# Kernel tuning notes

Measured on AMD Instinct MI355X. Metric: run time of the kernel, lower is better.

Reference implementation:

```python
import jax, jax.numpy as jnp
import numpy as np
from jax import lax

RADIUS = 32
STRIDE = RADIUS // 2
EPS = 1e-4
DN = ('NCHW', 'OIHW', 'NCHW')


def _upsample_bilinear_ac(x, H, W):
    # align_corners=True bilinear resize of NCHW x to (H, W), separable gather.
    b, c, h, w = x.shape
    ys = jnp.linspace(0.0, h - 1, H)
    xs = jnp.linspace(0.0, w - 1, W)
    y0 = jnp.floor(ys).astype(jnp.int32)
    y1 = jnp.minimum(y0 + 1, h - 1)
    wy = (ys - y0.astype(x.dtype)).astype(x.dtype)
    x0 = jnp.floor(xs).astype(jnp.int32)
    x1 = jnp.minimum(x0 + 1, w - 1)
    wx = (xs - x0.astype(x.dtype)).astype(x.dtype)
    rows = x[:, :, y0, :] * (1 - wy)[None, None, :, None] + x[:, :, y1, :] * wy[None, None, :, None]
    out = rows[:, :, :, x0] * (1 - wx) + rows[:, :, :, x1] * wx
    return out


def reference(guide, src, w1, w3):
    B, _, H, W = guide.shape
    f32 = guide.dtype

    def box3(x):  # depthwise strided box-sum (all-ones weights)
        return lax.conv_general_dilated(x, w3, (STRIDE, STRIDE), 'VALID',
                                        dimension_numbers=DN, feature_group_count=3)

    def box1(x):  # learned 1-channel strided conv
        return lax.conv_general_dilated(x, w1, (STRIDE, STRIDE), 'VALID',
                                        dimension_numbers=DN)

    gr, gg, gb = guide[:, 0:1], guide[:, 1:2], guide[:, 2:3]
    N = box1(jnp.ones_like(gr))                     # [B,1,h,w]
    mean_I = box3(guide) / N                        # [B,3,h,w]
    mIr, mIg, mIb = mean_I[:, 0:1], mean_I[:, 1:2], mean_I[:, 2:3]
    mean_p = box3(src) / N                          # [B,3,h,w]

    cov_r = box3(gr * src) / N - mIr * mean_p       # [B,3,h,w]
    cov_g = box3(gg * src) / N - mIg * mean_p
    cov_b = box3(gb * src) / N - mIb * mean_p

    v_rr = box1(gr * gr) / N - mIr * mIr + EPS
    v_rg = box1(gr * gg) / N - mIr * mIg
    v_rb = box1(gr * gb) / N - mIr * mIb
    v_gg = box1(gg * gg) / N - mIg * mIg + EPS
    v_gb = box1(gg * gb) / N - mIg * mIb
    v_bb = box1(gb * gb) / N - mIb * mIb + EPS

    det = (v_rr * v_gg * v_bb + v_rg * v_gb * v_rb + v_rb * v_rg * v_gb
           - v_rb * v_gg * v_rb - v_rg * v_rg * v_bb - v_rr * v_gb * v_gb)

    i_rr = (v_gg * v_bb - v_gb * v_gb) / det
    i_rg = -(v_rg * v_bb - v_rb * v_gb) / det
    i_rb = (v_rg * v_gb - v_rb * v_gg) / det
    i_gg = (v_rr * v_bb - v_rb * v_rb) / det
    i_gb = -(v_rr * v_gb - v_rb * v_rg) / det
    i_bb = (v_rr * v_gg - v_rg * v_rg) / det

    # inv_sigma: [B,3,3,h,w] (each i_* is [B,1,h,w] -> concat on channel)
    row_r = jnp.concatenate([i_rr, i_rg, i_rb], axis=1)
    row_g = jnp.concatenate([i_rg, i_gg, i_gb], axis=1)
    row_b = jnp.concatenate([i_rb, i_gb, i_bb], axis=1)
    inv_sigma = jnp.stack([row_r, row_g, row_b], axis=1)

    cov_Ip = jnp.stack([cov_r, cov_g, cov_b], axis=1)   # [B,3(i),3(c),h,w]
    A = jnp.einsum('bichw,bijhw->bjchw', cov_Ip, inv_sigma)  # [B,3(j),3(c),h,w]

    b_map = mean_p - A[:, 0] * mIr - A[:, 1] * mIg - A[:, 2] * mIb  # [B,3,h,w]

    h, w = A.shape[-2], A.shape[-1]
    mean_A = _upsample_bilinear_ac(A.reshape(B, 9, h, w), H, W).reshape(B, 3, 3, H, W)
    mean_b = _upsample_bilinear_ac(b_map, H, W)

    # q_c = sum_j A_{j,c} * guide_j + b_c
    return jnp.einsum('bjchw,bjhw->bchw', mean_A, guide) + mean_b


def setup_inputs() -> dict:
    key = jax.random.key(0)
    k1, k2, k3 = jax.random.split(key, 3)
    guide = jax.random.uniform(k1, (8, 3, 1024, 1024), dtype=jnp.float32)
    src = jax.random.uniform(k2, (8, 3, 1024, 1024), dtype=jnp.float32)
    w1 = jax.random.uniform(k3, (1, 1, RADIUS, RADIUS), dtype=jnp.float32)
    w3 = jnp.ones((3, 1, RADIUS, RADIUS), dtype=jnp.float32)
    return {"guide": guide, "src": src, "w1": w1, "w3": w3}
```

## Files before the change

### kernel.cpp

```cpp
#include <hip/hip_runtime.h>

#define HLO 63
#define HFULL 1024
#define GF_EPS 1e-4f
#define LOPLANE (HLO*HLO)
#define NQ 64
#define NSTAT 40

template<int CTRL>
__device__ __forceinline__ float dppadd(float v) {
    int r = __builtin_amdgcn_update_dpp(0, __float_as_int(v), CTRL, 0xF, 0xF, false);
    return v + __int_as_float(r);
}

__global__ __launch_bounds__(256) void gf_vstats(
    const float* __restrict__ guide, const float* __restrict__ src,
    const float* __restrict__ w1, float* __restrict__ hs)
{
    __shared__ float red[4][NSTAT][4];

    int bid = blockIdx.x;
    int cg = bid & 15;
    int qy = (bid >> 4) & 63;
    int b  = bid >> 10;
    int tid = threadIdx.x;
    int lane = tid & 63;
    int wv   = tid >> 6;

    int r   = lane & 3;
    int c4  = lane >> 2;
    int xin = (c4 & 3) * 4;
    int yin = wv * 4 + r;

    const size_t plane = (size_t)HFULL * HFULL;
    const float* g0 = guide + (size_t)b * 3 * plane
                    + (size_t)(qy * 16 + yin) * HFULL + cg * 64 + c4 * 4;
    const float* s0 = src   + (size_t)b * 3 * plane
                    + (size_t)(qy * 16 + yin) * HFULL + cg * 64 + c4 * 4;

    float4 vgr = *reinterpret_cast<const float4*>(g0);
    float4 vgg = *reinterpret_cast<const float4*>(g0 + plane);
    float4 vgb = *reinterpret_cast<const float4*>(g0 + 2 * plane);
    float4 vpr = *reinterpret_cast<const float4*>(s0);
    float4 vpg = *reinterpret_cast<const float4*>(s0 + plane);
    float4 vpb = *reinterpret_cast<const float4*>(s0 + 2 * plane);
    const float* wb = w1 + yin * 32 + xin;
    float4 w00 = *reinterpret_cast<const float4*>(wb);
    float4 w01 = *reinterpret_cast<const float4*>(wb + 16);
    float4 w10 = *reinterpret_cast<const float4*>(wb + 512);
    float4 w11 = *reinterpret_cast<const float4*>(wb + 528);

    const float* grf = reinterpret_cast<const float*>(&vgr);
    const float* ggf = reinterpret_cast<const float*>(&vgg);
    const float* gbf = reinterpret_cast<const float*>(&vgb);
    const float* prf = reinterpret_cast<const float*>(&vpr);
    const float* pgf = reinterpret_cast<const float*>(&vpg);
    const float* pbf = reinterpret_cast<const float*>(&vpb);
    const float* w00f = reinterpret_cast<const float*>(&w00);
    const float* w01f = reinterpret_cast<const float*>(&w01);
    const float* w10f = reinterpret_cast<const float*>(&w10);
    const float* w11f = reinterpret_cast<const float*>(&w11);

    float acc[NSTAT];
#pragma unroll
    for (int i = 0; i < NSTAT; i++) acc[i] = 0.f;

#pragma unroll
    for (int j = 0; j < 4; ++j) {
        float Gr = grf[j], Gg = ggf[j], Gb = gbf[j];
        float Pr = prf[j], Pg = pgf[j], Pb = pbf[j];
        float W00 = w00f[j], W01 = w01f[j], W10 = w10f[j], W11 = w11f[j];

        acc[0] += Gr;  acc[1] += Gg;  acc[2] += Gb;
        acc[3] += Pr;  acc[4] += Pg;  acc[5] += Pb;
        acc[6]  += Gr * Pr;  acc[7]  += Gr * Pg;  acc[8]  += Gr * Pb;
        acc[9]  += Gg * Pr;  acc[10] += Gg * Pg;  acc[11] += Gg * Pb;
        acc[12] += Gb * Pr;  acc[13] += Gb * Pg;  acc[14] += Gb * Pb;

        float RR = Gr * Gr, RG = Gr * Gg, RB = Gr * Gb;
        float GG = Gg * Gg, GB = Gg * Gb, BB = Gb * Gb;
        acc[15] += W00 * RR;  acc[16] += W01 * RR;  acc[17] += W10 * RR;  acc[18] += W11 * RR;
        acc[19] += W00 * RG;  acc[20] += W01 * RG;  acc[21] += W10 * RG;  acc[22] += W11 * RG;
        acc[23] += W00 * RB;  acc[24] += W01 * RB;  acc[25] += W10 * RB;  acc[26] += W11 * RB;
        acc[27] += W00 * GG;  acc[28] += W01 * GG;  acc[29] += W10 * GG;  acc[30] += W11 * GG;
        acc[31] += W00 * GB;  acc[32] += W01 * GB;  acc[33] += W10 * GB;  acc[34] += W11 * GB;
        acc[35] += W00 * BB;  acc[36] += W01 * BB;  acc[37] += W10 * BB;  acc[38] += W11 * BB;
        acc[39] += (W00 + W01) + (W10 + W11);
    }

#pragma unroll
    for (int i = 0; i < NSTAT; i++) {
        acc[i] = dppadd<0xB1>(acc[i]);
        acc[i] = dppadd<0x4E>(acc[i]);
        acc[i] += __shfl_xor(acc[i], 4, 64);
        acc[i] += __shfl_xor(acc[i], 8, 64);
    }

    if ((lane & 15) == 0) {
        int g = lane >> 4;
#pragma unroll
        for (int i = 0; i < NSTAT; i++)
            red[wv][i][g] = acc[i];
    }
    __syncthreads();

    if (tid < NSTAT * 4) {
        int stat = tid >> 2, g = tid & 3;
        float sum = red[0][stat][g] + red[1][stat][g]
                  + red[2][stat][g] + red[3][stat][g];
        hs[((size_t)(b * NQ + qy) * NSTAT + stat) * 64 + cg * 4 + g] = sum;
    }
}

__global__ __launch_bounds__(256) void gf_solve(
    const float* __restrict__ hs, float* __restrict__ ab)
{
    __shared__ float hl[2][NSTAT][64];

    int bid = blockIdx.x;
    int ly = bid % HLO;
    int b  = bid / HLO;
    int tid = threadIdx.x;

    const float4* sA = reinterpret_cast<const float4*>(
        hs + (size_t)(b * NQ + ly) * NSTAT * 64);
    const float4* sB = reinterpret_cast<const float4*>(
        hs + (size_t)(b * NQ + ly + 1) * NSTAT * 64);
    float4* dA = reinterpret_cast<float4*>(&hl[0][0][0]);
    float4* dB = reinterpret_cast<float4*>(&hl[1][0][0]);

    for (int i = tid; i < NSTAT * 16; i += 256) {
        dA[i] = sA[i];
        dB[i] = sB[i];
    }
    __syncthreads();

    if (tid >= HLO) return;
    int lx = tid;

    float s[15];
#pragma unroll
    for (int i = 0; i < 15; i++)
        s[i] = (hl[0][i][lx] + hl[0][i][lx + 1]) + (hl[1][i][lx] + hl[1][i][lx + 1]);

    float v[6];
#pragma unroll
    for (int p = 0; p < 6; p++) {
        int bs = 15 + p * 4;
        v[p] = hl[0][bs + 0][lx]
             + hl[0][bs + 1][lx + 1]
             + hl[1][bs + 2][lx]
             + hl[1][bs + 3][lx + 1];
    }
    float N = hl[0][39][lx];

    float inv_n = 1.f / N;
    float mI[3] = { s[0] * inv_n, s[1] * inv_n, s[2] * inv_n };
    float mp[3] = { s[3] * inv_n, s[4] * inv_n, s[5] * inv_n };

    float cov[3][3];
#pragma unroll
    for (int i = 0; i < 3; i++)
#pragma unroll
        for (int c = 0; c < 3; c++)
            cov[i][c] = s[6 + i * 3 + c] * inv_n - mI[i] * mp[c];

    float v_rr = v[0] * inv_n - mI[0] * mI[0] + GF_EPS;
    float v_rg = v[1] * inv_n - mI[0] * mI[1];
    float v_rb = v[2] * inv_n - mI[0] * mI[2];
    float v_gg = v[3] * inv_n - mI[1] * mI[1] + GF_EPS;
    float v_gb = v[4] * inv_n - mI[1] * mI[2];
    float v_bb = v[5] * inv_n - mI[2] * mI[2] + GF_EPS;

    float det = v_rr * v_gg * v_bb + v_rg * v_gb * v_rb + v_rb * v_rg * v_gb
              - v_rb * v_gg * v_rb - v_rg * v_rg * v_bb - v_rr * v_gb * v_gb;
    float invdet = 1.f / det;

    float i_rr =  (v_gg * v_bb - v_gb * v_gb) * invdet;
    float i_rg = -(v_rg * v_bb - v_rb * v_gb) * invdet;
    float i_rb =  (v_rg * v_gb - v_rb * v_gg) * invdet;
    float i_gg =  (v_rr * v_bb - v_rb * v_rb) * invdet;
    float i_gb = -(v_rr * v_gb - v_rb * v_rg) * invdet;
    float i_bb =  (v_rr * v_gg - v_rg * v_rg) * invdet;

    float inv[3][3] = { { i_rr, i_rg, i_rb },
                        { i_rg, i_gg, i_gb },
                        { i_rb, i_gb, i_bb } };

    float A[3][3];
#pragma unroll
    for (int j = 0; j < 3; j++)
#pragma unroll
        for (int c = 0; c < 3; c++)
            A[j][c] = inv[j][0] * cov[0][c] + inv[j][1] * cov[1][c] + inv[j][2] * cov[2][c];

    float bb_[3];
#pragma unroll
    for (int c = 0; c < 3; c++)
        bb_[c] = mp[c] - A[0][c] * mI[0] - A[1][c] * mI[1] - A[2][c] * mI[2];

    float* outp = ab + (size_t)b * 12 * LOPLANE + ly * HLO + lx;
#pragma unroll
    for (int j = 0; j < 3; j++)
#pragma unroll
        for (int c = 0; c < 3; c++)
            outp[(j * 3 + c) * LOPLANE] = A[j][c];
#pragma unroll
    for (int c = 0; c < 3; c++)
        outp[(9 + c) * LOPLANE] = bb_[c];
}

__global__ __launch_bounds__(256) void gf_apply(
    const float* __restrict__ guide, const float* __restrict__ ab,
    float* __restrict__ out)
{
    __shared__ float rl[12][64];

    int bid = blockIdx.x;
    int y = bid & 1023;
    int b = bid >> 10;
    int tid = threadIdx.x;

    const float scale = 62.0f / 1023.0f;
    float ty = (float)y * scale;
    int y0 = (int)ty;  if (y0 > 61) y0 = 61;
    float wy = ty - (float)y0;

    const float* abb = ab + (size_t)b * 12 * LOPLANE;
    for (int i = tid; i < 12 * 63; i += 256) {
        int p = i / 63, c = i - p * 63;
        const float* pp = abb + (size_t)p * LOPLANE + y0 * HLO + c;
        rl[p][c] = pp[0] * (1.f - wy) + pp[HLO] * wy;
    }
    __syncthreads();

    int x = 4 * tid;
    float t0 = (float)x * scale;
    int c0 = (int)t0;  if (c0 > 61) c0 = 61;

    bool  sel[4];
    float wx[4];
#pragma unroll
    for (int j = 0; j < 4; ++j) {
        float t = (float)(x + j) * scale;
        int x0 = (int)t;  if (x0 > 61) x0 = 61;
        sel[j] = (x0 > c0);
        wx[j]  = t - (float)x0;
    }

    float Av[12][4];
#pragma unroll
    for (int p = 0; p < 12; ++p) {
        float r0 = rl[p][c0], r1 = rl[p][c0 + 1], r2 = rl[p][c0 + 2];
#pragma unroll
        for (int j = 0; j < 4; ++j) {
            float a  = sel[j] ? r1 : r0;
            float bb = sel[j] ? r2 : r1;
            Av[p][j] = a + (bb - a) * wx[j];
        }
    }

    const size_t plane = (size_t)HFULL * HFULL;
    size_t goff = (size_t)b * 3 * plane + ((size_t)y << 10) + x;
    float4 vgr = *reinterpret_cast<const float4*>(guide + goff);
    float4 vgg = *reinterpret_cast<const float4*>(guide + goff + plane);
    float4 vgb = *reinterpret_cast<const float4*>(guide + goff + 2 * plane);
    const float* grf = reinterpret_cast<const float*>(&vgr);
    const float* ggf = reinterpret_cast<const float*>(&vgg);
    const float* gbf = reinterpret_cast<const float*>(&vgb);

#pragma unroll
    for (int c = 0; c < 3; ++c) {
        float4 o;
        float* of = reinterpret_cast<float*>(&o);
#pragma unroll
        for (int j = 0; j < 4; ++j)
            of[j] = Av[0 + c][j] * grf[j] + Av[3 + c][j] * ggf[j]
                  + Av[6 + c][j] * gbf[j] + Av[9 + c][j];
        *reinterpret_cast<float4*>(out + goff + (size_t)c * plane) = o;
    }
}

extern "C" void kernel_launch(void* const* d_in, const int* in_sizes, int n_in,
                              void* d_out, int out_size, void* d_ws, size_t ws_size,
                              hipStream_t stream) {
    const float* guide = (const float*)d_in[0];
    const float* src   = (const float*)d_in[1];
    const float* w1    = (const float*)d_in[2];
    float* out = (float*)d_out;

    float* ab = (float*)d_ws;
    float* hs = (float*)((char*)d_ws + (2 << 20));

    gf_vstats<<<8 * NQ * 16, 256, 0, stream>>>(guide, src, w1, hs);

    gf_solve<<<8 * HLO, 256, 0, stream>>>(hs, ab);

    gf_apply<<<8 * 1024, 256, 0, stream>>>(guide, ab, out);
}
```

Before: 86.52 us.

## Loop vstats over batches with prefetch, drop LDS reduction, sum quarters in solve

The stats kernel now launches 2048 blocks. Each block walks 4 batch images (b0, b0+2, ...) and prefetches the next image's guide/src float4s while it computes the current one. The per-block shared-memory reduction and __syncthreads are removed. Each wave writes its own quarter-row partial stats, and gf_solve sums the four quarters when it loads. This is meant to cut block count and sync overhead and to hide load latency, at the cost of 4x more partial-stat writes and extra reads in solve.

```diff
diff --git a/kernel.cpp b/kernel.cpp
--- a/kernel.cpp
+++ b/kernel.cpp
@@ -6,6 +6,7 @@
 #define LOPLANE (HLO*HLO)
 #define NQ 64
 #define NSTAT 40
+#define ITERS 4
 
 template<int CTRL>
 __device__ __forceinline__ float dppadd(float v) {
@@ -13,102 +14,117 @@
     return v + __int_as_float(r);
 }
 
-__global__ __launch_bounds__(256) void gf_vstats(
+__device__ __forceinline__ float4 f4add(float4 a, float4 b) {
+    return make_float4(a.x + b.x, a.y + b.y, a.z + b.z, a.w + b.w);
+}
+
+__global__ __launch_bounds__(256, 2) void gf_vstats(
     const float* __restrict__ guide, const float* __restrict__ src,
     const float* __restrict__ w1, float* __restrict__ hs)
 {
-    __shared__ float red[4][NSTAT][4];
-
     int bid = blockIdx.x;
     int cg = bid & 15;
     int qy = (bid >> 4) & 63;
-    int b  = bid >> 10;
+    int b0 = bid >> 10;
     int tid = threadIdx.x;
     int lane = tid & 63;
-    int wv   = tid >> 6;
-
-    int r   = lane & 3;
-    int c4  = lane >> 2;
+    int qtr  = tid >> 6;
+
+    int r   = lane >> 4;
+    int c4  = lane & 15;
+    int yin = qtr * 4 + r;
     int xin = (c4 & 3) * 4;
-    int yin = wv * 4 + r;
 
     const size_t plane = (size_t)HFULL * HFULL;
-    const float* g0 = guide + (size_t)b * 3 * plane
-                    + (size_t)(qy * 16 + yin) * HFULL + cg * 64 + c4 * 4;
-    const float* s0 = src   + (size_t)b * 3 * plane
-                    + (size_t)(qy * 16 + yin) * HFULL + cg * 64 + c4 * 4;
-
-    float4 vgr = *reinterpret_cast<const float4*>(g0);
-    float4 vgg = *reinterpret_cast<const float4*>(g0 + plane);
-    float4 vgb = *reinterpret_cast<const float4*>(g0 + 2 * plane);
-    float4 vpr = *reinterpret_cast<const float4*>(s0);
-    float4 vpg = *reinterpret_cast<const float4*>(s0 + plane);
-    float4 vpb = *reinterpret_cast<const float4*>(s0 + 2 * plane);
+    const size_t o0 = (size_t)(qy * 16 + yin) * HFULL + cg * 64 + c4 * 4;
+    const float* g0 = guide + (size_t)b0 * 3 * plane + o0;
+    const float* s0 = src   + (size_t)b0 * 3 * plane + o0;
+    const size_t bstep = (size_t)6 * plane;
+
     const float* wb = w1 + yin * 32 + xin;
     float4 w00 = *reinterpret_cast<const float4*>(wb);
     float4 w01 = *reinterpret_cast<const float4*>(wb + 16);
     float4 w10 = *reinterpret_cast<const float4*>(wb + 512);
     float4 w11 = *reinterpret_cast<const float4*>(wb + 528);
-
-    const float* grf = reinterpret_cast<const float*>(&vgr);
-    const float* ggf = reinterpret_cast<const float*>(&vgg);
-    const float* gbf = reinterpret_cast<const float*>(&vgb);
-    const float* prf = reinterpret_cast<const float*>(&vpr);
-    const float* pgf = reinterpret_cast<const float*>(&vpg);
-    const float* pbf = reinterpret_cast<const float*>(&vpb);
     const float* w00f = reinterpret_cast<const float*>(&w00);
     const float* w01f = reinterpret_cast<const float*>(&w01);
     const float* w10f = reinterpret_cast<const float*>(&w10);
     const float* w11f = reinterpret_cast<const float*>(&w11);
 
-    float acc[NSTAT];
-#pragma unroll
-    for (int i = 0; i < NSTAT; i++) acc[i] = 0.f;
-
-#pragma unroll
-    for (int j = 0; j < 4; ++j) {
-        float Gr = grf[j], Gg = ggf[j], Gb = gbf[j];
-        float Pr = prf[j], Pg = pgf[j], Pb = pbf[j];
-        float W00 = w00f[j], W01 = w01f[j], W10 = w10f[j], W11 = w11f[j];
-
-        acc[0] += Gr;  acc[1] += Gg;  acc[2] += Gb;
-        acc[3] += Pr;  acc[4] += Pg;  acc[5] += Pb;
-        acc[6]  += Gr * Pr;  acc[7]  += Gr * Pg;  acc[8]  += Gr * Pb;
-        acc[9]  += Gg * Pr;  acc[10] += Gg * Pg;  acc[11] += Gg * Pb;
-        acc[12] += Gb * Pr;  acc[13] += Gb * Pg;  acc[14] += Gb * Pb;
-
-        float RR = Gr * Gr, RG = Gr * Gg, RB = Gr * Gb;
-        float GG = Gg * Gg, GB = Gg * Gb, BB = Gb * Gb;
-        acc[15] += W00 * RR;  acc[16] += W01 * RR;  acc[17] += W10 * RR;  acc[18] += W11 * RR;
-        acc[19] += W00 * RG;  acc[20] += W01 * RG;  acc[21] += W10 * RG;  acc[22] += W11 * RG;
-        acc[23] += W00 * RB;  acc[24] += W01 * RB;  acc[25] += W10 * RB;  acc[26] += W11 * RB;
-        acc[27] += W00 * GG;  acc[28] += W01 * GG;  acc[29] += W10 * GG;  acc[30] += W11 * GG;
-        acc[31] += W00 * GB;  acc[32] += W01 * GB;  acc[33] += W10 * GB;  acc[34] += W11 * GB;
-        acc[35] += W00 * BB;  acc[36] += W01 * BB;  acc[37] += W10 * BB;  acc[38] += W11 * BB;
-        acc[39] += (W00 + W01) + (W10 + W11);
-    }
-
-#pragma unroll
-    for (int i = 0; i < NSTAT; i++) {
-        acc[i] = dppadd<0xB1>(acc[i]);
-        acc[i] = dppadd<0x4E>(acc[i]);
-        acc[i] += __shfl_xor(acc[i], 4, 64);
-        acc[i] += __shfl_xor(acc[i], 8, 64);
-    }
-
-    if ((lane & 15) == 0) {
-        int g = lane >> 4;
-#pragma unroll
-        for (int i = 0; i < NSTAT; i++)
-            red[wv][i][g] = acc[i];
-    }
-    __syncthreads();
-
-    if (tid < NSTAT * 4) {
-        int stat = tid >> 2, g = tid & 3;
-        float sum = red[0][stat][g] + red[1][stat][g]
-                  + red[2][stat][g] + red[3][stat][g];
-        hs[((size_t)(b * NQ + qy) * NSTAT + stat) * 64 + cg * 4 + g] = sum;
+    float4 A0 = *reinterpret_cast<const float4*>(g0);
+    float4 A1 = *reinterpret_cast<const float4*>(g0 + plane);
+    float4 A2 = *reinterpret_cast<const float4*>(g0 + 2 * plane);
+    float4 A3 = *reinterpret_cast<const float4*>(s0);
+    float4 A4 = *reinterpret_cast<const float4*>(s0 + plane);
+    float4 A5 = *reinterpret_cast<const float4*>(s0 + 2 * plane);
+
+#pragma unroll
+    for (int it = 0; it < ITERS; ++it) {
+        float4 B0 = A0, B1 = A1, B2 = A2, B3 = A3, B4 = A4, B5 = A5;
+        if (it + 1 < ITERS) {
+            const float* gn = g0 + (size_t)(it + 1) * bstep;
+            const float* sn = s0 + (size_t)(it + 1) * bstep;
+            B0 = *reinterpret_cast<const float4*>(gn);
+            B1 = *reinterpret_cast<const float4*>(gn + plane);
+            B2 = *reinterpret_cast<const float4*>(gn + 2 * plane);
+            B3 = *reinterpret_cast<const float4*>(sn);
+            B4 = *reinterpret_cast<const float4*>(sn + plane);
+            B5 = *reinterpret_cast<const float4*>(sn + 2 * plane);
+        }
+
+        const float* grf = reinterpret_cast<const float*>(&A0);
+        const float* ggf = reinterpret_cast<const float*>(&A1);
+        const float* gbf = reinterpret_cast<const float*>(&A2);
+        const float* prf = reinterpret_cast<const float*>(&A3);
+        const float* pgf = reinterpret_cast<const float*>(&A4);
+        const float* pbf = reinterpret_cast<const float*>(&A5);
+
+        float acc[NSTAT];
+#pragma unroll
+        for (int i = 0; i < NSTAT; i++) acc[i] = 0.f;
+
+#pragma unroll
+        for (int j = 0; j < 4; ++j) {
+            float Gr = grf[j], Gg = ggf[j], Gb = gbf[j];
+            float Pr = prf[j], Pg = pgf[j], Pb = pbf[j];
+            float W00 = w00f[j], W01 = w01f[j], W10 = w10f[j], W11 = w11f[j];
+
+            acc[0] += Gr;  acc[1] += Gg;  acc[2] += Gb;
+            acc[3] += Pr;  acc[4] += Pg;  acc[5] += Pb;
+            acc[6]  += Gr * Pr;  acc[7]  += Gr * Pg;  acc[8]  += Gr * Pb;
+            acc[9]  += Gg * Pr;  acc[10] += Gg * Pg;  acc[11] += Gg * Pb;
+            acc[12] += Gb * Pr;  acc[13] += Gb * Pg;  acc[14] += Gb * Pb;
+
+            float RR = Gr * Gr, RG = Gr * Gg, RB = Gr * Gb;
+            float GG = Gg * Gg, GB = Gg * Gb, BB = Gb * Gb;
+            acc[15] += W00 * RR;  acc[16] += W01 * RR;  acc[17] += W10 * RR;  acc[18] += W11 * RR;
+            acc[19] += W00 * RG;  acc[20] += W01 * RG;  acc[21] += W10 * RG;  acc[22] += W11 * RG;
+            acc[23] += W00 * RB;  acc[24] += W01 * RB;  acc[25] += W10 * RB;  acc[26] += W11 * RB;
+            acc[27] += W00 * GG;  acc[28] += W01 * GG;  acc[29] += W10 * GG;  acc[30] += W11 * GG;
+            acc[31] += W00 * GB;  acc[32] += W01 * GB;  acc[33] += W10 * GB;  acc[34] += W11 * GB;
+            acc[35] += W00 * BB;  acc[36] += W01 * BB;  acc[37] += W10 * BB;  acc[38] += W11 * BB;
+            acc[39] += (W00 + W01) + (W10 + W11);
+        }
+
+#pragma unroll
+        for (int i = 0; i < NSTAT; i++) {
+            acc[i] = dppadd<0xB1>(acc[i]);
+            acc[i] = dppadd<0x4E>(acc[i]);
+            acc[i] += __shfl_xor(acc[i], 16, 64);
+            acc[i] += __shfl_xor(acc[i], 32, 64);
+        }
+
+        if (lane < 16 && (lane & 3) == 0) {
+            int g = lane >> 2;
+            int b = b0 + 2 * it;
+            float* hp = hs + ((size_t)((b * NQ + qy) * 4 + qtr) * NSTAT) * 64
+                           + cg * 4 + g;
+#pragma unroll
+            for (int i = 0; i < NSTAT; i++)
+                hp[i * 64] = acc[i];
+        }
+
+        A0 = B0; A1 = B1; A2 = B2; A3 = B3; A4 = B4; A5 = B5;
     }
 }
 
@@ -122,16 +138,16 @@
     int b  = bid / HLO;
     int tid = threadIdx.x;
 
-    const float4* sA = reinterpret_cast<const float4*>(
-        hs + (size_t)(b * NQ + ly) * NSTAT * 64);
-    const float4* sB = reinterpret_cast<const float4*>(
-        hs + (size_t)(b * NQ + ly + 1) * NSTAT * 64);
+    const float4* qa = reinterpret_cast<const float4*>(
+        hs + (size_t)((b * NQ + ly) * 4) * NSTAT * 64);
+    const float4* qb = reinterpret_cast<const float4*>(
+        hs + (size_t)((b * NQ + ly + 1) * 4) * NSTAT * 64);
     float4* dA = reinterpret_cast<float4*>(&hl[0][0][0]);
     float4* dB = reinterpret_cast<float4*>(&hl[1][0][0]);
 
     for (int i = tid; i < NSTAT * 16; i += 256) {
-        dA[i] = sA[i];
-        dB[i] = sB[i];
+        dA[i] = f4add(f4add(qa[i], qa[i + 640]), f4add(qa[i + 1280], qa[i + 1920]));
+        dB[i] = f4add(f4add(qb[i], qb[i + 640]), f4add(qb[i + 1280], qb[i + 1920]));
     }
     __syncthreads();
 
@@ -292,7 +308,7 @@
     float* ab = (float*)d_ws;
     float* hs = (float*)((char*)d_ws + (2 << 20));
 
-    gf_vstats<<<8 * NQ * 16, 256, 0, stream>>>(guide, src, w1, hs);
+    gf_vstats<<<2048, 256, 0, stream>>>(guide, src, w1, hs);
 
     gf_solve<<<8 * HLO, 256, 0, stream>>>(hs, ab);
 
```

After: 101.9 us. +17.8%, slower.
